# Kernel tuning notes

Hardware: AMD Instinct MI355X
Metric: run time of the kernel (lower is better)

Reference implementation:

```python
import jax, jax.numpy as jnp
import numpy as np

N_NODES = 100000


def _gcn_conv(h, src, dst, norm, W, b, n):
    # linear transform then symmetric-normalized scatter-add aggregation
    hw = h @ W                                   # [N, out]
    msg = hw[src] * norm[:, None]                # [E+N, out] gathered messages
    out = jax.ops.segment_sum(msg, dst, num_segments=n)
    return out + b


def _self_loops_and_norm(edge_index, n):
    loop = jnp.arange(n, dtype=edge_index.dtype)
    src = jnp.concatenate([edge_index[0], loop])
    dst = jnp.concatenate([edge_index[1], loop])
    deg = jax.ops.segment_sum(jnp.ones_like(src, dtype=jnp.float32), dst, num_segments=n)
    dinv = jnp.where(deg > 0, jax.lax.rsqrt(jnp.maximum(deg, 1.0)), 0.0)
    norm = dinv[src] * dinv[dst]                 # D^-1/2 (A+I) D^-1/2 coefficients
    return src, dst, norm


def setup_inputs() -> dict:
    key = jax.random.key(0)
    k1, k2, k3, k4 = jax.random.split(key, 4)
    F_IN, H, C = 128, 64, 40
    x = jax.random.normal(k1, (N_NODES, F_IN), dtype=jnp.float32)
    edge_index = jax.random.randint(k2, (2, 3200000), 0, N_NODES, dtype=jnp.int64)
    s1 = 1.0 / np.sqrt(F_IN)
    s2 = 1.0 / np.sqrt(H)
    W1 = jax.random.uniform(k3, (F_IN, H), jnp.float32, -s1, s1)
    b1 = jnp.zeros((H,), jnp.float32)
    W2 = jax.random.uniform(k4, (H, C), jnp.float32, -s2, s2)
    b2 = jnp.zeros((C,), jnp.float32)
    return {"x": x, "edge_index": edge_index, "W1": W1, "b1": b1, "W2": W2, "b2": b2}


def reference(x, edge_index, W1, b1, W2, b2):
    n = x.shape[0]
    src, dst, norm = _self_loops_and_norm(edge_index, n)
    h = _gcn_conv(x, src, dst, norm, W1, b1, n)
    h = jax.nn.relu(h)
    # dropout(p=0.5) is identity in eval mode
    out = _gcn_conv(h, src, dst, norm, W2, b2, n)
    return jax.nn.log_softmax(out, axis=1)
```

## Files before the change

### kernel.cpp

```cpp
#include <hip/hip_runtime.h>
#include <math.h>

#define F_IN 128
#define HID  64
#define NCLS 40
#define PART_CHUNK 4096
#define CAP 4608
#define CAPX 768
#define MAXNB 1024
#define ASTRIDE 132

typedef _Float16 half8 __attribute__((ext_vector_type(8)));
typedef _Float16 half2t __attribute__((ext_vector_type(2)));
typedef float floatx4 __attribute__((ext_vector_type(4)));

__device__ inline half8 ld_half8_u8(const _Float16* p) {
    union { uint2 u[2]; half8 h; } r;
    r.u[0] = *(const uint2*)p;
    r.u[1] = *(const uint2*)(p + 4);
    return r.h;
}

__global__ __launch_bounds__(256) void fused_part_gemm1(const int* __restrict__ src,
                                                        const int* __restrict__ dst,
                                                        int* __restrict__ bCur,
                                                        int* __restrict__ pkBuf,
                                                        int E, int NB, int nPart,
                                                        const float* __restrict__ x,
                                                        const float* __restrict__ W1,
                                                        _Float16* __restrict__ h1, int n) {
    __shared__ __align__(16) char smem[2 * 64 * ASTRIDE * 2];
    int tid = threadIdx.x;
    if ((int)blockIdx.x < nPart) {
        int xcd = (int)blockIdx.x & 7;
        int* hcnt  = (int*)smem;
        int* hbase = (int*)smem + MAXNB;
        for (int i = tid; i < NB; i += 256) hcnt[i] = 0;
        __syncthreads();
        int e0 = blockIdx.x * PART_CHUNK;
        int s_[16], d_[16];
#pragma unroll
        for (int i = 0; i < 16; ++i) {
            int e = e0 + i * 256 + tid;
            if (e < E) {
                s_[i] = src[e]; d_[i] = dst[e];
                atomicAdd(&hcnt[d_[i] >> 7], 1);
            }
        }
        __syncthreads();
        for (int b = tid; b < NB; b += 256) {
            int c = hcnt[b];
            hbase[b] = c ? ((b * 8 + xcd) * CAPX + atomicAdd(&bCur[b * 8 + xcd], c)) : 0;
            hcnt[b] = 0;
        }
        __syncthreads();
#pragma unroll
        for (int i = 0; i < 16; ++i) {
            int e = e0 + i * 256 + tid;
            if (e < E) {
                int b = d_[i] >> 7;
                int loc = atomicAdd(&hcnt[b], 1);
                pkBuf[hbase[b] + loc] = (s_[i] << 7) | (d_[i] & 127);
            }
        }
    } else {
        _Float16* Ah = (_Float16*)smem;
        _Float16* Wt = Ah + 64 * ASTRIDE;
        int node0 = ((int)blockIdx.x - nPart) * 64;
#pragma unroll
        for (int i = 0; i < 8; ++i) {
            int f = (i * 256 + tid) * 4;
            int m = f >> 7, k = f & 127;
            float4 v = (node0 + m < n) ? ((const float4*)(x + (size_t)(node0 + m) * F_IN))[k >> 2]
                                       : make_float4(0.f, 0.f, 0.f, 0.f);
            _Float16* p = &Ah[m * ASTRIDE + k];
            p[0] = (_Float16)v.x; p[1] = (_Float16)v.y; p[2] = (_Float16)v.z; p[3] = (_Float16)v.w;
        }
#pragma unroll
        for (int i = 0; i < 32; ++i) {
            int f = i * 256 + tid;
            int k = f >> 6, nn = f & 63;
            Wt[nn * ASTRIDE + k] = (_Float16)W1[f];
        }
        __syncthreads();
        int wave = tid >> 6, lane = tid & 63;
        int m0 = wave * 16;
        int col = lane & 15, quad = lane >> 4;
        floatx4 acc[4] = {{0,0,0,0},{0,0,0,0},{0,0,0,0},{0,0,0,0}};
#pragma unroll
        for (int kk = 0; kk < 4; ++kk) {
            int kbase = kk * 32 + quad * 8;
            half8 a = ld_half8_u8(&Ah[(m0 + col) * ASTRIDE + kbase]);
#pragma unroll
            for (int t = 0; t < 4; ++t) {
                half8 b = ld_half8_u8(&Wt[(t * 16 + col) * ASTRIDE + kbase]);
                acc[t] = __builtin_amdgcn_mfma_f32_16x16x32_f16(a, b, acc[t], 0, 0, 0);
            }
        }
#pragma unroll
        for (int t = 0; t < 4; ++t)
#pragma unroll
            for (int r = 0; r < 4; ++r) {
                int node = node0 + m0 + quad * 4 + r;
                if (node < n) h1[(size_t)node * HID + t * 16 + col] = (_Float16)acc[t][r];
            }
    }
}

__global__ __launch_bounds__(256) void scan_buckets(const int* __restrict__ bCur,
                                                    int* __restrict__ bBase, int NB, int E) {
    __shared__ int part[256];
    int tid = threadIdx.x;
    int v[4]; int sum = 0;
#pragma unroll
    for (int k = 0; k < 4; ++k) {
        int i = tid * 4 + k;
        int s = 0;
        if (i < NB) {
#pragma unroll
            for (int x = 0; x < 8; ++x) s += bCur[i * 8 + x];
        }
        v[k] = s;
        sum += s;
    }
    part[tid] = sum; __syncthreads();
    for (int off = 1; off < 256; off <<= 1) {
        int t = (tid >= off) ? part[tid - off] : 0;
        __syncthreads();
        part[tid] += t;
        __syncthreads();
    }
    int base = part[tid] - sum;
#pragma unroll
    for (int k = 0; k < 4; ++k) {
        int i = tid * 4 + k;
        if (i < NB) bBase[i] = base;
        base += v[k];
    }
    if (tid == 255) bBase[NB] = E;
}

__global__ __launch_bounds__(256) void bucket_finalize(const int* __restrict__ bCur,
                                                       const int* __restrict__ bBase,
                                                       const int* __restrict__ pkBuf,
                                                       int* __restrict__ ptr,
                                                       float* __restrict__ dinv,
                                                       int* __restrict__ sIdx,
                                                       _Float16* __restrict__ h1,
                                                       int n, int E) {
    __shared__ int cnt128[128];
    __shared__ int sc[128];
    __shared__ int cur[128];
    __shared__ float sdinv[128];
    __shared__ int segoff[9];
    __shared__ int ebuf[CAP];
    __shared__ int stage[CAP];
    int b = blockIdx.x;
    int node0 = b << 7;
    int tid = threadIdx.x;
    if (tid < 128) cnt128[tid] = 0;
    if (tid == 0) {
        int o = 0;
#pragma unroll
        for (int x = 0; x < 8; ++x) { segoff[x] = o; o += bCur[b * 8 + x]; }
        segoff[8] = o;
    }
    __syncthreads();
    int cnt = segoff[8];
    int dbase = bBase[b];
    for (int x = 0; x < 8; ++x) {
        int off = segoff[x], len = segoff[x + 1] - off;
        const int* s = pkBuf + (size_t)(b * 8 + x) * CAPX;
        for (int j = tid; j < len; j += 256) {
            int p = s[j];
            ebuf[off + j] = p;
            atomicAdd(&cnt128[p & 127], 1);
        }
    }
    __syncthreads();
    int v = (tid < 128) ? cnt128[tid] : 0;
    if (tid < 128) sc[tid] = v;
    __syncthreads();
    for (int off = 1; off < 128; off <<= 1) {
        int t = (tid < 128 && tid >= off) ? sc[tid - off] : 0;
        __syncthreads();
        if (tid < 128) sc[tid] += t;
        __syncthreads();
    }
    if (tid < 128) {
        cur[tid] = sc[tid] - v;
        float dv = rsqrtf((float)v + 1.0f);
        sdinv[tid] = dv;
        int node = node0 + tid;
        if (node < n) {
            ptr[node] = dbase + sc[tid] - v;
            dinv[node] = dv;
        }
    }
    if (tid == 0 && b == gridDim.x - 1) ptr[n] = E;
    __syncthreads();
    for (int j = tid; j < cnt; j += 256) {
        int p = ebuf[j];
        int pos = atomicAdd(&cur[p & 127], 1);
        stage[pos] = p >> 7;
    }
    __syncthreads();
    for (int j = tid; j < cnt; j += 256)
        sIdx[dbase + j] = stage[j];
#pragma unroll
    for (int pass = 0; pass < 4; ++pass) {
        int idx = pass * 256 + tid;
        int nd = node0 + (idx >> 3);
        if (nd < n) {
            float dv = sdinv[idx >> 3];
            half8* p = (half8*)(h1 + (size_t)nd * HID) + (idx & 7);
            half8 hv = *p;
#pragma unroll
            for (int j = 0; j < 8; ++j) hv[j] = (_Float16)((float)hv[j] * dv);
            *p = hv;
        }
    }
}

template<bool RELU>
__global__ __launch_bounds__(256) void gather4(const int* __restrict__ ptr,
                                               const int* __restrict__ sIdx,
                                               const float* __restrict__ dinv,
                                               const _Float16* __restrict__ hin,
                                               const float* __restrict__ bias,
                                               _Float16* __restrict__ hout, int n) {
    int tid = threadIdx.x, wave = tid >> 6, lane = tid & 63;
    int ng   = lane >> 4;
    int slot = (lane >> 3) & 1;
    int fq   = lane & 7;
    int node = blockIdx.x * 16 + wave * 4 + ng;
    bool valid = node < n;
    int nodeC = valid ? node : 0;
    int beg = ptr[nodeC];
    int end = valid ? ptr[nodeC + 1] : beg;
    float di = dinv[nodeC];
    float a0[8] = {0,0,0,0,0,0,0,0}, a1[8] = {0,0,0,0,0,0,0,0};

    if (slot == 0 && valid) {
        half8 v = *(const half8*)(hin + nodeC * HID + fq * 8);
#pragma unroll
        for (int j = 0; j < 8; ++j) a0[j] = (float)v[j];
    }
    const _Float16 ONE = (_Float16)1.0f, ZEROH = (_Float16)0.0f;
    if (beg < end) {
        int ja0 = beg + slot, jb0 = ja0 + 2, jc0 = ja0 + 4, jd0 = ja0 + 6;
        bool va = ja0 < end, vb = jb0 < end, vc = jc0 < end, vd = jd0 < end;
        int sa0 = sIdx[va ? ja0 : beg];
        int sb0 = sIdx[vb ? jb0 : beg];
        int sc0 = sIdx[vc ? jc0 : beg];
        int sd0 = sIdx[vd ? jd0 : beg];
        int ja1 = ja0 + 8, jb1 = jb0 + 8, jc1 = jc0 + 8, jd1 = jd0 + 8;
        bool va1 = ja1 < end, vb1 = jb1 < end, vc1 = jc1 < end, vd1 = jd1 < end;
        int sa1 = sIdx[va1 ? ja1 : beg];
        int sb1 = sIdx[vb1 ? jb1 : beg];
        int sc1 = sIdx[vc1 ? jc1 : beg];
        int sd1 = sIdx[vd1 ? jd1 : beg];
        half8 ra = *(const half8*)(hin + (size_t)sa0 * HID + fq * 8);
        half8 rb = *(const half8*)(hin + (size_t)sb0 * HID + fq * 8);
        half8 rc = *(const half8*)(hin + (size_t)sc0 * HID + fq * 8);
        half8 rd = *(const half8*)(hin + (size_t)sd0 * HID + fq * 8);
        for (int j0 = beg; j0 < end; j0 += 8) {
            half8 ra2 = *(const half8*)(hin + (size_t)sa1 * HID + fq * 8);
            half8 rb2 = *(const half8*)(hin + (size_t)sb1 * HID + fq * 8);
            half8 rc2 = *(const half8*)(hin + (size_t)sc1 * HID + fq * 8);
            half8 rd2 = *(const half8*)(hin + (size_t)sd1 * HID + fq * 8);
            int ja2 = j0 + 16 + slot, jb2 = ja2 + 2, jc2 = ja2 + 4, jd2 = ja2 + 6;
            bool va2 = ja2 < end, vb2 = jb2 < end, vc2 = jc2 < end, vd2 = jd2 < end;
            int sa2 = sIdx[va2 ? ja2 : beg];
            int sb2 = sIdx[vb2 ? jb2 : beg];
            int sc2 = sIdx[vc2 ? jc2 : beg];
            int sd2 = sIdx[vd2 ? jd2 : beg];
#if __has_builtin(__builtin_amdgcn_fdot2)
            half2t wab = { va ? ONE : ZEROH, vb ? ONE : ZEROH };
            half2t wcd = { vc ? ONE : ZEROH, vd ? ONE : ZEROH };
#pragma unroll
            for (int j = 0; j < 8; ++j) {
                half2t pab = { ra[j], rb[j] };
                half2t pcd = { rc[j], rd[j] };
                a0[j] = __builtin_amdgcn_fdot2(pab, wab, a0[j], false);
                a1[j] = __builtin_amdgcn_fdot2(pcd, wcd, a1[j], false);
            }
#else
            float wa = va ? 1.f : 0.f, wb = vb ? 1.f : 0.f, wc = vc ? 1.f : 0.f, wd = vd ? 1.f : 0.f;
#pragma unroll
            for (int j = 0; j < 8; ++j) {
                a0[j] = fmaf((float)ra[j], wa, a0[j]);
                a0[j] = fmaf((float)rb[j], wb, a0[j]);
                a1[j] = fmaf((float)rc[j], wc, a1[j]);
                a1[j] = fmaf((float)rd[j], wd, a1[j]);
            }
#endif
            ra = ra2; rb = rb2; rc = rc2; rd = rd2;
            va = va1; vb = vb1; vc = vc1; vd = vd1;
            sa1 = sa2; sb1 = sb2; sc1 = sc2; sd1 = sd2;
            va1 = va2; vb1 = vb2; vc1 = vc2; vd1 = vd2;
        }
    }
#pragma unroll
    for (int j = 0; j < 8; ++j) {
        a0[j] += a1[j];
        a0[j] += __shfl_xor(a0[j], 8, 64);
    }
    if (slot == 0 && valid) {
        union { half8 h; uint4 u; } o;
#pragma unroll
        for (int j = 0; j < 8; ++j) {
            float v = di * a0[j];
            if (RELU) v = fmaxf(v + bias[fq * 8 + j], 0.f) * di;
            o.h[j] = (_Float16)v;
        }
        *(uint4*)(hout + nodeC * HID + fq * 8) = o.u;
    }
}

#define GSTRIDE 72
__global__ __launch_bounds__(256) void gemm2_mfma_logsm(const _Float16* __restrict__ g,
                                                        const float* __restrict__ W2,
                                                        const float* __restrict__ b2,
                                                        float* __restrict__ out, int n) {
    __shared__ _Float16 gt[64 * GSTRIDE];
    __shared__ _Float16 wt[48 * GSTRIDE];
    int tid = threadIdx.x;
    int node0 = blockIdx.x * 64;
#pragma unroll
    for (int i = 0; i < 2; ++i) {
        int f = (i * 256 + tid) * 8;
        int m = f >> 6, k = f & 63;
        union { uint4 u; half8 h; } v;
        if (node0 + m < n) v.u = *(const uint4*)(g + (size_t)(node0 + m) * HID + k);
        else v.u = make_uint4(0, 0, 0, 0);
        *(uint4*)&gt[m * GSTRIDE + k] = v.u;
    }
#pragma unroll
    for (int i = 0; i < 12; ++i) {
        int f = i * 256 + tid;
        int c = f >> 6, k = f & 63;
        wt[c * GSTRIDE + k] = (c < NCLS) ? (_Float16)W2[k * NCLS + c] : (_Float16)0.f;
    }
    __syncthreads();

    int wave = tid >> 6, lane = tid & 63;
    int m0 = wave * 16;
    int col = lane & 15, quad = lane >> 4;
    floatx4 acc[3] = {{0,0,0,0},{0,0,0,0},{0,0,0,0}};
#pragma unroll
    for (int kk = 0; kk < 2; ++kk) {
        int kbase = kk * 32 + quad * 8;
        half8 a = *(const half8*)&gt[(m0 + col) * GSTRIDE + kbase];
#pragma unroll
        for (int t = 0; t < 3; ++t) {
            half8 b = *(const half8*)&wt[(t * 16 + col) * GSTRIDE + kbase];
            acc[t] = __builtin_amdgcn_mfma_f32_16x16x32_f16(a, b, acc[t], 0, 0, 0);
        }
    }
    float bb[3];
#pragma unroll
    for (int t = 0; t < 3; ++t) {
        int c = t * 16 + col;
        bb[t] = (c < NCLS) ? b2[c] : 0.f;
    }
#pragma unroll
    for (int r = 0; r < 4; ++r) {
        int node = node0 + m0 + quad * 4 + r;
        float v0 = acc[0][r] + bb[0];
        float v1 = acc[1][r] + bb[1];
        float v2 = (col < 8) ? acc[2][r] + bb[2] : -INFINITY;
        float m = fmaxf(fmaxf(v0, v1), v2);
#pragma unroll
        for (int off = 1; off < 16; off <<= 1) m = fmaxf(m, __shfl_xor(m, off, 64));
        float s = expf(v0 - m) + expf(v1 - m) + ((col < 8) ? expf(v2 - m) : 0.f);
#pragma unroll
        for (int off = 1; off < 16; off <<= 1) s += __shfl_xor(s, off, 64);
        float ls = logf(s);
        if (node < n) {
            float* op = out + (size_t)node * NCLS;
            op[col]      = v0 - m - ls;
            op[16 + col] = v1 - m - ls;
            if (col < 8) op[32 + col] = v2 - m - ls;
        }
    }
}

extern "C" void kernel_launch(void* const* d_in, const int* in_sizes, int n_in,
                              void* d_out, int out_size, void* d_ws, size_t ws_size,
                              hipStream_t stream) {
    const float* x  = (const float*)d_in[0];
    const int*   ei = (const int*)d_in[1];
    const float* W1 = (const float*)d_in[2];
    const float* b1 = (const float*)d_in[3];
    const float* W2 = (const float*)d_in[4];
    const float* b2 = (const float*)d_in[5];
    float* out = (float*)d_out;

    int n = in_sizes[0] / F_IN;
    int E = in_sizes[1] / 2;
    const int* src = ei;
    const int* dst = ei + E;
    int NB = (n + 127) >> 7;
    int nPart = (E + PART_CHUNK - 1) / PART_CHUNK;
    int nGemm1 = (n + 63) / 64;

    char* ws = (char*)d_ws;
    const size_t MB = 1024 * 1024;
    int*      bCur  = (int*)  (ws);
    int*      bBase = (int*)  (ws + 64 * 1024);
    int*      ptr   = (int*)  (ws + 128 * 1024);
    float*    dinv  = (float*)(ws + 1 * MB);
    int*      sIdx  = (int*)     (ws + 2 * MB);
    _Float16* bufA  = (_Float16*)(ws + 15 * MB);
    int*      pkBuf = (int*)     (ws + 28 * MB);
    _Float16* bufB  = (_Float16*)(ws + 28 * MB);

    hipMemsetAsync(bCur, 0, (size_t)NB * 8 * sizeof(int), stream);
    fused_part_gemm1<<<nPart + nGemm1, 256, 0, stream>>>(src, dst, bCur, pkBuf, E, NB, nPart,
                                                         x, W1, bufA, n);
    scan_buckets<<<1, 256, 0, stream>>>(bCur, bBase, NB, E);
    bucket_finalize<<<NB, 256, 0, stream>>>(bCur, bBase, pkBuf, ptr, dinv, sIdx, bufA, n, E);

    gather4<true ><<<(n + 15) / 16, 256, 0, stream>>>(ptr, sIdx, dinv, bufA, b1, bufB, n);
    gather4<false><<<(n + 15) / 16, 256, 0, stream>>>(ptr, sIdx, dinv, bufB, b1, bufA, n);
    gemm2_mfma_logsm<<<(n + 63) / 64, 256, 0, stream>>>(bufA, W2, b2, out, n);
}
```

Measured before the change: 298.6 us.

## Fuse second-layer GEMM and log-softmax into the final gather kernel

The separate gemm2_mfma_logsm kernel is merged into the second gather pass. Each block stages its 16 aggregated rows and the fp16-converted W2 in shared memory, and wave 0 then runs the MFMA projection and log-softmax, writing the output directly. This removes one launch and the global write and re-read of the 64-wide hidden buffer. In exchange, every gather block reloads W2, adds a block barrier, and only one of four waves does the GEMM epilogue.

```diff
diff --git a/kernel.cpp b/kernel.cpp
--- a/kernel.cpp
+++ b/kernel.cpp
@@ -9,6 +9,7 @@
 #define CAPX 768
 #define MAXNB 1024
 #define ASTRIDE 132
+#define GSTRIDE 72
 
 typedef _Float16 half8 __attribute__((ext_vector_type(8)));
 typedef _Float16 half2t __attribute__((ext_vector_type(2)));
@@ -228,7 +229,12 @@
                                                const float* __restrict__ dinv,
                                                const _Float16* __restrict__ hin,
                                                const float* __restrict__ bias,
-                                               _Float16* __restrict__ hout, int n) {
+                                               _Float16* __restrict__ hout,
+                                               const float* __restrict__ W2,
+                                               const float* __restrict__ b2,
+                                               float* __restrict__ out, int n) {
+    __shared__ _Float16 gt[16 * GSTRIDE];
+    __shared__ _Float16 wt[48 * GSTRIDE];
     int tid = threadIdx.x, wave = tid >> 6, lane = tid & 63;
     int ng   = lane >> 4;
     int slot = (lane >> 3) & 1;
@@ -240,6 +246,15 @@
     int end = valid ? ptr[nodeC + 1] : beg;
     float di = dinv[nodeC];
     float a0[8] = {0,0,0,0,0,0,0,0}, a1[8] = {0,0,0,0,0,0,0,0};
+
+    if (!RELU) {
+#pragma unroll
+        for (int i = 0; i < 12; ++i) {
+            int f = i * 256 + tid;
+            int c = f >> 6, k = f & 63;
+            wt[c * GSTRIDE + k] = (c < NCLS) ? (_Float16)W2[k * NCLS + c] : (_Float16)0.f;
+        }
+    }
 
     if (slot == 0 && valid) {
         half8 v = *(const half8*)(hin + nodeC * HID + fq * 8);
@@ -306,82 +321,66 @@
         a0[j] += a1[j];
         a0[j] += __shfl_xor(a0[j], 8, 64);
     }
-    if (slot == 0 && valid) {
-        union { half8 h; uint4 u; } o;
-#pragma unroll
-        for (int j = 0; j < 8; ++j) {
-            float v = di * a0[j];
-            if (RELU) v = fmaxf(v + bias[fq * 8 + j], 0.f) * di;
-            o.h[j] = (_Float16)v;
-        }
-        *(uint4*)(hout + nodeC * HID + fq * 8) = o.u;
-    }
-}
-
-#define GSTRIDE 72
-__global__ __launch_bounds__(256) void gemm2_mfma_logsm(const _Float16* __restrict__ g,
-                                                        const float* __restrict__ W2,
-                                                        const float* __restrict__ b2,
-                                                        float* __restrict__ out, int n) {
-    __shared__ _Float16 gt[64 * GSTRIDE];
-    __shared__ _Float16 wt[48 * GSTRIDE];
-    int tid = threadIdx.x;
-    int node0 = blockIdx.x * 64;
-#pragma unroll
-    for (int i = 0; i < 2; ++i) {
-        int f = (i * 256 + tid) * 8;
-        int m = f >> 6, k = f & 63;
-        union { uint4 u; half8 h; } v;
-        if (node0 + m < n) v.u = *(const uint4*)(g + (size_t)(node0 + m) * HID + k);
-        else v.u = make_uint4(0, 0, 0, 0);
-        *(uint4*)&gt[m * GSTRIDE + k] = v.u;
-    }
-#pragma unroll
-    for (int i = 0; i < 12; ++i) {
-        int f = i * 256 + tid;
-        int c = f >> 6, k = f & 63;
-        wt[c * GSTRIDE + k] = (c < NCLS) ? (_Float16)W2[k * NCLS + c] : (_Float16)0.f;
-    }
-    __syncthreads();
-
-    int wave = tid >> 6, lane = tid & 63;
-    int m0 = wave * 16;
-    int col = lane & 15, quad = lane >> 4;
-    floatx4 acc[3] = {{0,0,0,0},{0,0,0,0},{0,0,0,0}};
-#pragma unroll
-    for (int kk = 0; kk < 2; ++kk) {
-        int kbase = kk * 32 + quad * 8;
-        half8 a = *(const half8*)&gt[(m0 + col) * GSTRIDE + kbase];
-#pragma unroll
-        for (int t = 0; t < 3; ++t) {
-            half8 b = *(const half8*)&wt[(t * 16 + col) * GSTRIDE + kbase];
-            acc[t] = __builtin_amdgcn_mfma_f32_16x16x32_f16(a, b, acc[t], 0, 0, 0);
-        }
-    }
-    float bb[3];
-#pragma unroll
-    for (int t = 0; t < 3; ++t) {
-        int c = t * 16 + col;
-        bb[t] = (c < NCLS) ? b2[c] : 0.f;
-    }
-#pragma unroll
-    for (int r = 0; r < 4; ++r) {
-        int node = node0 + m0 + quad * 4 + r;
-        float v0 = acc[0][r] + bb[0];
-        float v1 = acc[1][r] + bb[1];
-        float v2 = (col < 8) ? acc[2][r] + bb[2] : -INFINITY;
-        float m = fmaxf(fmaxf(v0, v1), v2);
-#pragma unroll
-        for (int off = 1; off < 16; off <<= 1) m = fmaxf(m, __shfl_xor(m, off, 64));
-        float s = expf(v0 - m) + expf(v1 - m) + ((col < 8) ? expf(v2 - m) : 0.f);
-#pragma unroll
-        for (int off = 1; off < 16; off <<= 1) s += __shfl_xor(s, off, 64);
-        float ls = logf(s);
-        if (node < n) {
-            float* op = out + (size_t)node * NCLS;
-            op[col]      = v0 - m - ls;
-            op[16 + col] = v1 - m - ls;
-            if (col < 8) op[32 + col] = v2 - m - ls;
+
+    if (RELU) {
+        if (slot == 0 && valid) {
+            union { half8 h; uint4 u; } o;
+#pragma unroll
+            for (int j = 0; j < 8; ++j) {
+                float v = di * a0[j];
+                v = fmaxf(v + bias[fq * 8 + j], 0.f) * di;
+                o.h[j] = (_Float16)v;
+            }
+            *(uint4*)(hout + nodeC * HID + fq * 8) = o.u;
+        }
+    } else {
+        if (slot == 0) {
+            int row = wave * 4 + ng;
+#pragma unroll
+            for (int j = 0; j < 8; ++j)
+                gt[row * GSTRIDE + fq * 8 + j] = (_Float16)(di * a0[j]);
+        }
+        __syncthreads();
+        if (wave == 0) {
+            int col = lane & 15, quad = lane >> 4;
+            floatx4 acc[3] = {{0,0,0,0},{0,0,0,0},{0,0,0,0}};
+#pragma unroll
+            for (int kk = 0; kk < 2; ++kk) {
+                int kbase = kk * 32 + quad * 8;
+                half8 a = *(const half8*)&gt[col * GSTRIDE + kbase];
+#pragma unroll
+                for (int t = 0; t < 3; ++t) {
+                    half8 b = *(const half8*)&wt[(t * 16 + col) * GSTRIDE + kbase];
+                    acc[t] = __builtin_amdgcn_mfma_f32_16x16x32_f16(a, b, acc[t], 0, 0, 0);
+                }
+            }
+            float bb[3];
+#pragma unroll
+            for (int t = 0; t < 3; ++t) {
+                int c = t * 16 + col;
+                bb[t] = (c < NCLS) ? b2[c] : 0.f;
+            }
+            int nodeB = blockIdx.x * 16;
+#pragma unroll
+            for (int r = 0; r < 4; ++r) {
+                int nd = nodeB + quad * 4 + r;
+                float v0 = acc[0][r] + bb[0];
+                float v1 = acc[1][r] + bb[1];
+                float v2 = (col < 8) ? acc[2][r] + bb[2] : -INFINITY;
+                float m = fmaxf(fmaxf(v0, v1), v2);
+#pragma unroll
+                for (int off = 1; off < 16; off <<= 1) m = fmaxf(m, __shfl_xor(m, off, 64));
+                float s = expf(v0 - m) + expf(v1 - m) + ((col < 8) ? expf(v2 - m) : 0.f);
+#pragma unroll
+                for (int off = 1; off < 16; off <<= 1) s += __shfl_xor(s, off, 64);
+                float ls = logf(s);
+                if (nd < n) {
+                    float* op = out + (size_t)nd * NCLS;
+                    op[col]      = v0 - m - ls;
+                    op[16 + col] = v1 - m - ls;
+                    if (col < 8) op[32 + col] = v2 - m - ls;
+                }
+            }
         }
     }
 }
@@ -422,7 +421,8 @@
     scan_buckets<<<1, 256, 0, stream>>>(bCur, bBase, NB, E);
     bucket_finalize<<<NB, 256, 0, stream>>>(bCur, bBase, pkBuf, ptr, dinv, sIdx, bufA, n, E);
 
-    gather4<true ><<<(n + 15) / 16, 256, 0, stream>>>(ptr, sIdx, dinv, bufA, b1, bufB, n);
-    gather4<false><<<(n + 15) / 16, 256, 0, stream>>>(ptr, sIdx, dinv, bufB, b1, bufA, n);
-    gemm2_mfma_logsm<<<(n + 63) / 64, 256, 0, stream>>>(bufA, W2, b2, out, n);
-}
+    gather4<true ><<<(n + 15) / 16, 256, 0, stream>>>(ptr, sIdx, dinv, bufA, b1, bufB,
+                                                      W2, b2, out, n);
+    gather4<false><<<(n + 15) / 16, 256, 0, stream>>>(ptr, sIdx, dinv, bufB, b1, bufB,
+                                                      W2, b2, out, n);
+}
```

New measurement: 297.9 us. Within noise of the previous version (-0.2%).
